# Kernel tuning notes

Measured on AMD Instinct MI355X. Metric: run time of the kernel, lower is better.

Reference implementation:

```python
import jax, jax.numpy as jnp
import numpy as np

E = 768   # embed_size
H = 64    # head_embed_size
B = 8
T = 4096  # == ctx_size


def setup_inputs() -> dict:
    key = jax.random.key(0)
    k1, k2, k3, k4 = jax.random.split(key, 4)
    inputs = jax.random.normal(k1, (B, T, E), dtype=jnp.float32)
    # Linear weights stored as (E, H) so projection is x @ W
    scale = 1.0 / np.sqrt(E)
    Wq = jax.random.uniform(k2, (E, H), dtype=jnp.float32, minval=-scale, maxval=scale)
    Wk = jax.random.uniform(k3, (E, H), dtype=jnp.float32, minval=-scale, maxval=scale)
    Wv = jax.random.uniform(k4, (E, H), dtype=jnp.float32, minval=-scale, maxval=scale)
    return {"inputs": inputs, "Wq": Wq, "Wk": Wk, "Wv": Wv}


def reference(inputs, Wq, Wk, Wv):
    Tlen = inputs.shape[1]
    q = inputs @ Wq  # (B,T,H)
    k = inputs @ Wk  # (B,T,H)
    v = inputs @ Wv  # (B,T,H)
    # NOTE: original module does NOT scale by 1/sqrt(H) — faithful reproduction.
    scores = jnp.einsum('bqh,bkh->bqk', q, k)  # (B,T,T)
    causal = jnp.tril(jnp.ones((Tlen, Tlen), dtype=bool))
    scores = jnp.where(causal, scores, -jnp.inf)
    attn = jax.nn.softmax(scores, axis=-1)
    # dropout=0 -> identity
    out = jnp.einsum('bqk,bkh->bqh', attn, v)  # (B,T,H)
    return out
```

## Files before the change

kernel.cpp:

```cpp
#include <hip/hip_runtime.h>
#include <hip/hip_bf16.h>

#define E_DIM 768
#define H_DIM 64
#define B_SZ 8
#define T_SZ 4096
#define BT (B_SZ * T_SZ)

typedef __attribute__((ext_vector_type(8))) short short8;
typedef __attribute__((ext_vector_type(4))) float floatx4;

#define RAWBAR() __asm__ volatile("s_waitcnt lgkmcnt(0)\n\ts_barrier" ::: "memory")

static __device__ __forceinline__ unsigned short bf1(float a) {
    __hip_bfloat16 h = __float2bfloat16(a);
    unsigned short u; __builtin_memcpy(&u, &h, 2); return u;
}
static __device__ __forceinline__ unsigned int pk2(float a, float b) {
    __hip_bfloat162 h = __float22bfloat162_rn(float2{a, b});
    unsigned int u; __builtin_memcpy(&u, &h, 4); return u;
}

__global__ __launch_bounds__(256) void prep_w(
    const float* __restrict__ Wq, const float* __restrict__ Wk,
    const float* __restrict__ Wv, unsigned short* __restrict__ Wt)
{
    __shared__ float Ls[64][65];
    const int nt = blockIdx.x;
    const int kc = blockIdx.y;
    const float* __restrict__ W = (nt == 0) ? Wq : (nt == 1) ? Wk : Wv;
    const float scl = (nt == 0) ? 1.44269504088896f : 1.0f;
    const int t = threadIdx.x;
    const int k0 = kc * 64;

#pragma unroll
    for (int it = 0; it < 16; ++it) {
        const int kk = (t >> 6) + it * 4;
        Ls[kk][t & 63] = W[(size_t)(k0 + kk) * H_DIM + (t & 63)];
    }
    __syncthreads();

#pragma unroll
    for (int it = 0; it < 4; ++it) {
        const int nl = (t >> 4) + it * 16;
        const int kl = (t & 15) * 4;
        unsigned int u[2];
        u[0] = pk2(Ls[kl + 0][nl] * scl, Ls[kl + 1][nl] * scl);
        u[1] = pk2(Ls[kl + 2][nl] * scl, Ls[kl + 3][nl] * scl);
        *(uint2*)(Wt + (size_t)(nt * 64 + nl) * E_DIM + k0 + kl) = *(uint2*)u;
    }
}

__global__ __launch_bounds__(768) void proj_mfma(
    const float* __restrict__ X, const unsigned short* __restrict__ Wt,
    unsigned short* __restrict__ Qb, unsigned short* __restrict__ Kb,
    unsigned short* __restrict__ Vtb)
{
    __shared__ unsigned short Xs[2][16][776];

    const int tid  = threadIdx.x;
    const int wave = tid >> 6, lane = tid & 63;
    const int row  = lane & 15, quad = lane >> 4;
    const int m0   = blockIdx.x * 128;

    short8 bfr[24];
    {
        const unsigned short* wp = Wt + (size_t)(wave * 16 + row) * E_DIM + quad * 8;
#pragma unroll
        for (int ks = 0; ks < 24; ++ks) bfr[ks] = *(const short8*)(wp + ks * 32);
    }

    const int srow = tid & 15;
    const int sc   = tid >> 4;
    const float* __restrict__ xbase = X + (size_t)(m0 + srow) * E_DIM + sc * 16;

    float4 fx[4];
#define LDX(mt)                                                               \
    {                                                                         \
        const float* p = xbase + (size_t)(mt) * 16 * E_DIM;                   \
        fx[0] = *(const float4*)(p);     fx[1] = *(const float4*)(p + 4);     \
        fx[2] = *(const float4*)(p + 8); fx[3] = *(const float4*)(p + 12);    \
    }
#define STX(buf)                                                              \
    {                                                                         \
        unsigned int tmp[8];                                                  \
        tmp[0] = pk2(fx[0].x, fx[0].y); tmp[1] = pk2(fx[0].z, fx[0].w);       \
        tmp[2] = pk2(fx[1].x, fx[1].y); tmp[3] = pk2(fx[1].z, fx[1].w);       \
        tmp[4] = pk2(fx[2].x, fx[2].y); tmp[5] = pk2(fx[2].z, fx[2].w);       \
        tmp[6] = pk2(fx[3].x, fx[3].y); tmp[7] = pk2(fx[3].z, fx[3].w);       \
        *(int4*)&Xs[buf][srow][sc * 16]     = *(int4*)&tmp[0];                \
        *(int4*)&Xs[buf][srow][sc * 16 + 8] = *(int4*)&tmp[4];                \
    }

    LDX(0); STX(0); LDX(1);
    RAWBAR();

    const int g  = wave >> 2;
    const int h  = (wave & 3) * 16 + row;
    unsigned short* __restrict__ OQK = (g == 0) ? Qb : Kb;
    const int bb = m0 >> 12;

    int cur = 0;
    for (int mt = 0; mt < 8; ++mt) {
        if (mt < 7) STX(cur ^ 1);
        if (mt < 6) LDX(mt + 2);

        floatx4 a0 = (floatx4)0.0f, a1 = (floatx4)0.0f;
        floatx4 a2 = (floatx4)0.0f, a3 = (floatx4)0.0f;
#pragma unroll
        for (int ks = 0; ks < 6; ++ks) {
            const short8 f0 = *(const short8*)&Xs[cur][row][(ks * 4 + 0) * 32 + quad * 8];
            const short8 f1 = *(const short8*)&Xs[cur][row][(ks * 4 + 1) * 32 + quad * 8];
            const short8 f2 = *(const short8*)&Xs[cur][row][(ks * 4 + 2) * 32 + quad * 8];
            const short8 f3 = *(const short8*)&Xs[cur][row][(ks * 4 + 3) * 32 + quad * 8];
            a0 = __builtin_amdgcn_mfma_f32_16x16x32_bf16(f0, bfr[ks * 4 + 0], a0, 0, 0, 0);
            a1 = __builtin_amdgcn_mfma_f32_16x16x32_bf16(f1, bfr[ks * 4 + 1], a1, 0, 0, 0);
            a2 = __builtin_amdgcn_mfma_f32_16x16x32_bf16(f2, bfr[ks * 4 + 2], a2, 0, 0, 0);
            a3 = __builtin_amdgcn_mfma_f32_16x16x32_bf16(f3, bfr[ks * 4 + 3], a3, 0, 0, 0);
        }
        floatx4 acc;
#pragma unroll
        for (int r = 0; r < 4; ++r) acc[r] = (a0[r] + a1[r]) + (a2[r] + a3[r]);

        const int mr = m0 + mt * 16 + quad * 4;
        if (g < 2) {
#pragma unroll
            for (int r = 0; r < 4; ++r)
                OQK[(size_t)(mr + r) * H_DIM + h] = bf1(acc[r]);
        } else {
            const int t0 = mr & 4095;
            unsigned int u[2];
            u[0] = pk2(acc[0], acc[1]); u[1] = pk2(acc[2], acc[3]);
            *(uint2*)(Vtb + ((size_t)bb * H_DIM + h) * T_SZ + t0) = *(uint2*)u;
        }

        RAWBAR();
        cur ^= 1;
    }
#undef LDX
#undef STX
}

__global__ __launch_bounds__(256, 6) void attn_mfma(
    const unsigned short* __restrict__ Qb,
    const unsigned short* __restrict__ Kb,
    const unsigned short* __restrict__ Vtb,
    float* __restrict__ Opart, float* __restrict__ lpart,
    float* __restrict__ Out)
{
    __shared__ __align__(16) unsigned short KV[2][64][72];
    __shared__ float lc[4][16];

    const int lb = blockIdx.x;
    const int b  = lb & 7;
    const int s  = lb >> 3;
    int qq, c, m;
    if (s < 128)      { m = 4; qq = 96 + (s >> 2); c = s & 3; }
    else if (s < 224) { m = 3; const int t = s - 128; const int t3 = t / 3; qq = 64 + t3; c = t - t3 * 3; }
    else if (s < 288) { m = 2; const int t = s - 224; qq = 32 + (t >> 1); c = t & 1; }
    else              { m = 1; qq = s - 288; c = 0; }
    const int ntot = (qq >> 1) + 1;
    const int k0t  = (c * ntot) / m;
    const int k1t  = ((c + 1) * ntot) / m;
    const int ktd  = ntot - 1;
    const int n    = k1t - k0t;
    const bool split = (m > 1);

    const int tid  = threadIdx.x;
    const int wave = tid >> 6, lane = tid & 63;
    const int col  = lane & 15, quad = lane >> 4;
    const int wq   = wave >> 1;
    const int wk   = wave & 1;

    const size_t base = (size_t)b * T_SZ * H_DIM;
    const int q0  = qq * 32;

    short8 qf0, qf1;
    {
        const unsigned short* qp = Qb + base + (size_t)(q0 + wq * 16 + col) * H_DIM + quad * 8;
        qf0 = *(const short8*)(qp);
        qf1 = *(const short8*)(qp + 32);
    }

    floatx4 o[4];
#pragma unroll
    for (int i = 0; i < 4; ++i) o[i] = (floatx4)0.0f;
    float lp = 0.0f;

    const int krow = tid >> 2, kcol = (tid & 3) * 16;
    const int kprow = (krow & 32) + ((krow >> 2) & 1) * 16 + ((krow & 31) >> 3) * 4 + (krow & 3);
    const unsigned short* __restrict__ Ksrc = Kb + base + (size_t)krow * H_DIM + kcol;
    const unsigned short* __restrict__ Vsrc = Vtb + ((size_t)b * H_DIM + krow) * T_SZ + kcol;

    int4 kr0, kr1, vr0, vr1;
#define LDKV(t)                                                          \
    {                                                                    \
        const unsigned short* kp = Ksrc + (size_t)(t) * 64 * H_DIM;      \
        kr0 = *(const int4*)kp; kr1 = *(const int4*)(kp + 8);            \
        const unsigned short* vp = Vsrc + (t) * 64;                      \
        vr0 = *(const int4*)vp; vr1 = *(const int4*)(vp + 8);            \
    }
#define STKV()                                                           \
    {                                                                    \
        *(int4*)&KV[0][kprow][kcol] = kr0; *(int4*)&KV[0][kprow][kcol + 8] = kr1; \
        *(int4*)&KV[1][krow][kcol] = vr0; *(int4*)&KV[1][krow][kcol + 8] = vr1; \
    }

    LDKV(k0t);
    STKV();
    if (n > 1) LDKV(k0t + 1);
    RAWBAR();

    for (int i = 0; i < n; ++i) {
        const int kt = k0t + i;

        floatx4 a0 = (floatx4)0.0f, a1 = (floatx4)0.0f;
        __builtin_amdgcn_s_setprio(1);
        {
            const unsigned short* kp0 = &KV[0][wk * 32 + col][quad * 8];
            const unsigned short* kp1 = &KV[0][wk * 32 + 16 + col][quad * 8];
            a0 = __builtin_amdgcn_mfma_f32_16x16x32_bf16(*(const short8*)(kp0),      qf0, a0, 0, 0, 0);
            a1 = __builtin_amdgcn_mfma_f32_16x16x32_bf16(*(const short8*)(kp1),      qf0, a1, 0, 0, 0);
            a0 = __builtin_amdgcn_mfma_f32_16x16x32_bf16(*(const short8*)(kp0 + 32), qf1, a0, 0, 0, 0);
            a1 = __builtin_amdgcn_mfma_f32_16x16x32_bf16(*(const short8*)(kp1 + 32), qf1, a1, 0, 0, 0);
        }
        __builtin_amdgcn_s_setprio(0);

        if (kt == ktd) {
            const int qg = q0 + wq * 16 + col;
            const int kb = kt * 64 + wk * 32 + quad * 8;
#pragma unroll
            for (int r = 0; r < 4; ++r) {
                if (kb + r > qg)     a0[r] = -1e30f;
                if (kb + 4 + r > qg) a1[r] = -1e30f;
            }
        }

        const float p0 = exp2f(a0[0]), p1 = exp2f(a0[1]), p2 = exp2f(a0[2]), p3 = exp2f(a0[3]);
        const float p4 = exp2f(a1[0]), p5 = exp2f(a1[1]), p6 = exp2f(a1[2]), p7 = exp2f(a1[3]);
        lp += ((p0 + p1) + (p2 + p3)) + ((p4 + p5) + (p6 + p7));
        unsigned int u0, u1, u2, u3;
        __asm__("v_cvt_pk_bf16_f32 %0, %1, %2" : "=v"(u0) : "v"(p0), "v"(p1));
        __asm__("v_cvt_pk_bf16_f32 %0, %1, %2" : "=v"(u1) : "v"(p2), "v"(p3));
        __asm__("v_cvt_pk_bf16_f32 %0, %1, %2" : "=v"(u2) : "v"(p4), "v"(p5));
        __asm__("v_cvt_pk_bf16_f32 %0, %1, %2" : "=v"(u3) : "v"(p6), "v"(p7));
        union { unsigned int u[4]; short8 v; } pu;
        pu.u[0] = u0; pu.u[1] = u1; pu.u[2] = u2; pu.u[3] = u3;
        const short8 pa = pu.v;

        __builtin_amdgcn_s_setprio(1);
#pragma unroll
        for (int d = 0; d < 4; ++d) {
            const short8 vb = *(const short8*)(&KV[1][d * 16 + col][wk * 32 + quad * 8]);
            o[d] = __builtin_amdgcn_mfma_f32_16x16x32_bf16(pa, vb, o[d], 0, 0, 0);
        }
        __builtin_amdgcn_s_setprio(0);

        RAWBAR();
        if (i + 1 < n) {
            STKV();
            if (i + 2 < n) LDKV(kt + 2);
        }
        RAWBAR();
    }

    lp += __shfl_xor(lp, 16);
    lp += __shfl_xor(lp, 32);
    if (quad == 0) lc[wave][col] = lp;
    __syncthreads();

    float* __restrict__ Oc = (float*)&KV[0][0][0];
#pragma unroll
    for (int r = 0; r < 4; ++r)
#pragma unroll
        for (int d = 0; d < 4; ++d)
            Oc[((wave * 16) + quad * 4 + r) * 64 + d * 16 + col] = o[d][r];
    __syncthreads();

    {
        const int orow = tid >> 3;
        const int d0   = (tid & 7) * 8;
        const int rl   = orow & 15;
        const int wb   = (orow >> 4) * 2;
        const float* p0 = &Oc[((wb * 16) + rl) * 64 + d0];
        const float* p1 = &Oc[(((wb + 1) * 16) + rl) * 64 + d0];
        const float lsum = lc[wb][rl] + lc[wb + 1][rl];
        float4 a0 = *(const float4*)(p0);
        float4 a1 = *(const float4*)(p0 + 4);
        const float4 b0 = *(const float4*)(p1);
        const float4 b1 = *(const float4*)(p1 + 4);
        a0.x += b0.x; a0.y += b0.y; a0.z += b0.z; a0.w += b0.w;
        a1.x += b1.x; a1.y += b1.y; a1.z += b1.z; a1.w += b1.w;
        if (!split) {
            const float inv = 1.0f / lsum;
            a0.x *= inv; a0.y *= inv; a0.z *= inv; a0.w *= inv;
            a1.x *= inv; a1.y *= inv; a1.z *= inv; a1.w *= inv;
            float* op = Out + base + (size_t)(q0 + orow) * H_DIM + d0;
            *(float4*)(op)     = a0;
            *(float4*)(op + 4) = a1;
        } else {
            const int pidx = (b * 96 + (qq - 32)) * 4 + c;
            float* op = Opart + ((size_t)pidx * 32 + orow) * 64 + d0;
            *(float4*)(op)     = a0;
            *(float4*)(op + 4) = a1;
            if ((tid & 7) == 0) lpart[pidx * 32 + orow] = lsum;
        }
    }
#undef LDKV
#undef STKV
}

__global__ __launch_bounds__(256) void attn_combine(
    const float* __restrict__ Opart, const float* __restrict__ lpart,
    float* __restrict__ Out)
{
    const int qi  = blockIdx.x;
    const int b   = blockIdx.y;
    const int qq  = 32 + qi;
    const int m   = (qq < 64) ? 2 : (qq < 96) ? 3 : 4;
    const int tid = threadIdx.x;
    const int orow = tid >> 3;
    const int d0   = (tid & 7) * 8;
    const int p0   = (b * 96 + qi) * 4;

    float4 a0 = {0.f, 0.f, 0.f, 0.f}, a1 = {0.f, 0.f, 0.f, 0.f};
    float l = 0.0f;
    for (int j = 0; j < m; ++j) {
        const float* P = Opart + ((size_t)(p0 + j) * 32 + orow) * 64 + d0;
        const float4 b0 = *(const float4*)(P);
        const float4 b1 = *(const float4*)(P + 4);
        a0.x += b0.x; a0.y += b0.y; a0.z += b0.z; a0.w += b0.w;
        a1.x += b1.x; a1.y += b1.y; a1.z += b1.z; a1.w += b1.w;
        l += lpart[(p0 + j) * 32 + orow];
    }
    const float inv = 1.0f / l;
    a0.x *= inv; a0.y *= inv; a0.z *= inv; a0.w *= inv;
    a1.x *= inv; a1.y *= inv; a1.z *= inv; a1.w *= inv;

    float* op = Out + ((size_t)b * T_SZ + qq * 32 + orow) * H_DIM + d0;
    *(float4*)(op)     = a0;
    *(float4*)(op + 4) = a1;
}

extern "C" void kernel_launch(void* const* d_in, const int* in_sizes, int n_in,
                              void* d_out, int out_size, void* d_ws, size_t ws_size,
                              hipStream_t stream) {
    const float* X  = (const float*)d_in[0];
    const float* Wq = (const float*)d_in[1];
    const float* Wk = (const float*)d_in[2];
    const float* Wv = (const float*)d_in[3];

    unsigned short* Wt  = (unsigned short*)d_ws;
    unsigned short* Qb  = Wt + (size_t)192 * E_DIM;
    unsigned short* Kb  = Qb + (size_t)BT * H_DIM;
    unsigned short* Vtb = Kb + (size_t)BT * H_DIM;
    float* Opart = (float*)(Vtb + (size_t)BT * H_DIM);
    float* lpart = Opart + (size_t)3072 * 32 * 64;

    prep_w<<<dim3(3, 12), 256, 0, stream>>>(Wq, Wk, Wv, Wt);
    proj_mfma<<<256, 768, 0, stream>>>(X, Wt, Qb, Kb, Vtb);
    attn_mfma<<<2560, 256, 0, stream>>>(Qb, Kb, Vtb, Opart, lpart, (float*)d_out);
    attn_combine<<<dim3(96, 8), 256, 0, stream>>>(Opart, lpart, (float*)d_out);
}
```

Before: 214.1 us.

## Grow attention query tile to 64 rows with each wave covering the full key tile

Each block now handles 64 query rows instead of 32, and each of the four waves owns 16 query rows across the whole 64-key tile. Each K/V tile loaded into shared memory is therefore reused by twice as many queries, and the cross-wave LDS reduction of partial outputs and row sums goes away, since each wave writes its rows directly. The split-K schedule is rebuilt for 64 query tiles with up to 6 chunks, and the grid and combine kernel are resized to match. The trade-off is fewer blocks (1632), more per-wave work and registers, and a lower occupancy hint of 5.

```diff
diff --git a/kernel.cpp b/kernel.cpp
--- a/kernel.cpp
+++ b/kernel.cpp
@@ -141,7 +141,7 @@
 #undef STX
 }
 
-__global__ __launch_bounds__(256, 6) void attn_mfma(
+__global__ __launch_bounds__(256, 5) void attn_mfma(
     const unsigned short* __restrict__ Qb,
     const unsigned short* __restrict__ Kb,
     const unsigned short* __restrict__ Vtb,
@@ -149,17 +149,18 @@
     float* __restrict__ Out)
 {
     __shared__ __align__(16) unsigned short KV[2][64][72];
-    __shared__ float lc[4][16];
 
     const int lb = blockIdx.x;
     const int b  = lb & 7;
     const int s  = lb >> 3;
     int qq, c, m;
-    if (s < 128)      { m = 4; qq = 96 + (s >> 2); c = s & 3; }
-    else if (s < 224) { m = 3; const int t = s - 128; const int t3 = t / 3; qq = 64 + t3; c = t - t3 * 3; }
-    else if (s < 288) { m = 2; const int t = s - 224; qq = 32 + (t >> 1); c = t & 1; }
-    else              { m = 1; qq = s - 288; c = 0; }
-    const int ntot = (qq >> 1) + 1;
+    if (s < 24)       { m = 6; qq = 60 + s / 6;                        c = s % 6; }
+    else if (s < 84)  { m = 5; const int i = s - 24;  qq = 48 + i / 5;    c = i % 5; }
+    else if (s < 132) { m = 4; const int i = s - 84;  qq = 36 + (i >> 2); c = i & 3; }
+    else if (s < 168) { m = 3; const int i = s - 132; qq = 24 + i / 3;    c = i % 3; }
+    else if (s < 192) { m = 2; const int i = s - 168; qq = 12 + (i >> 1); c = i & 1; }
+    else              { m = 1; qq = s - 192; c = 0; }
+    const int ntot = qq + 1;
     const int k0t  = (c * ntot) / m;
     const int k1t  = ((c + 1) * ntot) / m;
     const int ktd  = ntot - 1;
@@ -167,13 +168,12 @@
     const bool split = (m > 1);
 
     const int tid  = threadIdx.x;
-    const int wave = tid >> 6, lane = tid & 63;
+    const int wq   = tid >> 6;
+    const int lane = tid & 63;
     const int col  = lane & 15, quad = lane >> 4;
-    const int wq   = wave >> 1;
-    const int wk   = wave & 1;
 
     const size_t base = (size_t)b * T_SZ * H_DIM;
-    const int q0  = qq * 32;
+    const int q0  = qq * 64;
 
     short8 qf0, qf1;
     {
@@ -214,47 +214,50 @@
     for (int i = 0; i < n; ++i) {
         const int kt = k0t + i;
 
-        floatx4 a0 = (floatx4)0.0f, a1 = (floatx4)0.0f;
-        __builtin_amdgcn_s_setprio(1);
-        {
-            const unsigned short* kp0 = &KV[0][wk * 32 + col][quad * 8];
-            const unsigned short* kp1 = &KV[0][wk * 32 + 16 + col][quad * 8];
-            a0 = __builtin_amdgcn_mfma_f32_16x16x32_bf16(*(const short8*)(kp0),      qf0, a0, 0, 0, 0);
-            a1 = __builtin_amdgcn_mfma_f32_16x16x32_bf16(*(const short8*)(kp1),      qf0, a1, 0, 0, 0);
-            a0 = __builtin_amdgcn_mfma_f32_16x16x32_bf16(*(const short8*)(kp0 + 32), qf1, a0, 0, 0, 0);
-            a1 = __builtin_amdgcn_mfma_f32_16x16x32_bf16(*(const short8*)(kp1 + 32), qf1, a1, 0, 0, 0);
-        }
-        __builtin_amdgcn_s_setprio(0);
-
-        if (kt == ktd) {
-            const int qg = q0 + wq * 16 + col;
-            const int kb = kt * 64 + wk * 32 + quad * 8;
-#pragma unroll
-            for (int r = 0; r < 4; ++r) {
-                if (kb + r > qg)     a0[r] = -1e30f;
-                if (kb + 4 + r > qg) a1[r] = -1e30f;
+#pragma unroll
+        for (int j = 0; j < 2; ++j) {
+            floatx4 a0 = (floatx4)0.0f, a1 = (floatx4)0.0f;
+            __builtin_amdgcn_s_setprio(1);
+            {
+                const unsigned short* kp0 = &KV[0][j * 32 + col][quad * 8];
+                const unsigned short* kp1 = &KV[0][j * 32 + 16 + col][quad * 8];
+                a0 = __builtin_amdgcn_mfma_f32_16x16x32_bf16(*(const short8*)(kp0),      qf0, a0, 0, 0, 0);
+                a1 = __builtin_amdgcn_mfma_f32_16x16x32_bf16(*(const short8*)(kp1),      qf0, a1, 0, 0, 0);
+                a0 = __builtin_amdgcn_mfma_f32_16x16x32_bf16(*(const short8*)(kp0 + 32), qf1, a0, 0, 0, 0);
+                a1 = __builtin_amdgcn_mfma_f32_16x16x32_bf16(*(const short8*)(kp1 + 32), qf1, a1, 0, 0, 0);
             }
-        }
-
-        const float p0 = exp2f(a0[0]), p1 = exp2f(a0[1]), p2 = exp2f(a0[2]), p3 = exp2f(a0[3]);
-        const float p4 = exp2f(a1[0]), p5 = exp2f(a1[1]), p6 = exp2f(a1[2]), p7 = exp2f(a1[3]);
-        lp += ((p0 + p1) + (p2 + p3)) + ((p4 + p5) + (p6 + p7));
-        unsigned int u0, u1, u2, u3;
-        __asm__("v_cvt_pk_bf16_f32 %0, %1, %2" : "=v"(u0) : "v"(p0), "v"(p1));
-        __asm__("v_cvt_pk_bf16_f32 %0, %1, %2" : "=v"(u1) : "v"(p2), "v"(p3));
-        __asm__("v_cvt_pk_bf16_f32 %0, %1, %2" : "=v"(u2) : "v"(p4), "v"(p5));
-        __asm__("v_cvt_pk_bf16_f32 %0, %1, %2" : "=v"(u3) : "v"(p6), "v"(p7));
-        union { unsigned int u[4]; short8 v; } pu;
-        pu.u[0] = u0; pu.u[1] = u1; pu.u[2] = u2; pu.u[3] = u3;
-        const short8 pa = pu.v;
-
-        __builtin_amdgcn_s_setprio(1);
-#pragma unroll
-        for (int d = 0; d < 4; ++d) {
-            const short8 vb = *(const short8*)(&KV[1][d * 16 + col][wk * 32 + quad * 8]);
-            o[d] = __builtin_amdgcn_mfma_f32_16x16x32_bf16(pa, vb, o[d], 0, 0, 0);
-        }
-        __builtin_amdgcn_s_setprio(0);
+            __builtin_amdgcn_s_setprio(0);
+
+            if (kt == ktd) {
+                const int qg = q0 + wq * 16 + col;
+                const int kb = kt * 64 + j * 32 + quad * 8;
+#pragma unroll
+                for (int r = 0; r < 4; ++r) {
+                    if (kb + r > qg)     a0[r] = -1e30f;
+                    if (kb + 4 + r > qg) a1[r] = -1e30f;
+                }
+            }
+
+            const float p0 = exp2f(a0[0]), p1 = exp2f(a0[1]), p2 = exp2f(a0[2]), p3 = exp2f(a0[3]);
+            const float p4 = exp2f(a1[0]), p5 = exp2f(a1[1]), p6 = exp2f(a1[2]), p7 = exp2f(a1[3]);
+            lp += ((p0 + p1) + (p2 + p3)) + ((p4 + p5) + (p6 + p7));
+            unsigned int u0, u1, u2, u3;
+            __asm__("v_cvt_pk_bf16_f32 %0, %1, %2" : "=v"(u0) : "v"(p0), "v"(p1));
+            __asm__("v_cvt_pk_bf16_f32 %0, %1, %2" : "=v"(u1) : "v"(p2), "v"(p3));
+            __asm__("v_cvt_pk_bf16_f32 %0, %1, %2" : "=v"(u2) : "v"(p4), "v"(p5));
+            __asm__("v_cvt_pk_bf16_f32 %0, %1, %2" : "=v"(u3) : "v"(p6), "v"(p7));
+            union { unsigned int u[4]; short8 v; } pu;
+            pu.u[0] = u0; pu.u[1] = u1; pu.u[2] = u2; pu.u[3] = u3;
+            const short8 pa = pu.v;
+
+            __builtin_amdgcn_s_setprio(1);
+#pragma unroll
+            for (int d = 0; d < 4; ++d) {
+                const short8 vb = *(const short8*)(&KV[1][d * 16 + col][j * 32 + quad * 8]);
+                o[d] = __builtin_amdgcn_mfma_f32_16x16x32_bf16(pa, vb, o[d], 0, 0, 0);
+            }
+            __builtin_amdgcn_s_setprio(0);
+        }
 
         RAWBAR();
         if (i + 1 < n) {
@@ -266,45 +269,28 @@
 
     lp += __shfl_xor(lp, 16);
     lp += __shfl_xor(lp, 32);
-    if (quad == 0) lc[wave][col] = lp;
-    __syncthreads();
-
-    float* __restrict__ Oc = (float*)&KV[0][0][0];
-#pragma unroll
-    for (int r = 0; r < 4; ++r)
-#pragma unroll
-        for (int d = 0; d < 4; ++d)
-            Oc[((wave * 16) + quad * 4 + r) * 64 + d * 16 + col] = o[d][r];
-    __syncthreads();
-
-    {
-        const int orow = tid >> 3;
-        const int d0   = (tid & 7) * 8;
-        const int rl   = orow & 15;
-        const int wb   = (orow >> 4) * 2;
-        const float* p0 = &Oc[((wb * 16) + rl) * 64 + d0];
-        const float* p1 = &Oc[(((wb + 1) * 16) + rl) * 64 + d0];
-        const float lsum = lc[wb][rl] + lc[wb + 1][rl];
-        float4 a0 = *(const float4*)(p0);
-        float4 a1 = *(const float4*)(p0 + 4);
-        const float4 b0 = *(const float4*)(p1);
-        const float4 b1 = *(const float4*)(p1 + 4);
-        a0.x += b0.x; a0.y += b0.y; a0.z += b0.z; a0.w += b0.w;
-        a1.x += b1.x; a1.y += b1.y; a1.z += b1.z; a1.w += b1.w;
-        if (!split) {
-            const float inv = 1.0f / lsum;
-            a0.x *= inv; a0.y *= inv; a0.z *= inv; a0.w *= inv;
-            a1.x *= inv; a1.y *= inv; a1.z *= inv; a1.w *= inv;
-            float* op = Out + base + (size_t)(q0 + orow) * H_DIM + d0;
-            *(float4*)(op)     = a0;
-            *(float4*)(op + 4) = a1;
-        } else {
-            const int pidx = (b * 96 + (qq - 32)) * 4 + c;
-            float* op = Opart + ((size_t)pidx * 32 + orow) * 64 + d0;
-            *(float4*)(op)     = a0;
-            *(float4*)(op + 4) = a1;
-            if ((tid & 7) == 0) lpart[pidx * 32 + orow] = lsum;
-        }
+    float lr[4];
+#pragma unroll
+    for (int r = 0; r < 4; ++r) lr[r] = __shfl(lp, quad * 4 + r);
+
+    if (!split) {
+        float* op = Out + base + (size_t)(q0 + wq * 16 + quad * 4) * H_DIM;
+#pragma unroll
+        for (int r = 0; r < 4; ++r) {
+            const float inv = 1.0f / lr[r];
+#pragma unroll
+            for (int d = 0; d < 4; ++d)
+                op[(size_t)r * H_DIM + d * 16 + col] = o[d][r] * inv;
+        }
+    } else {
+        const int pidx = (b * 64 + qq) * 6 + c;
+        float* op = Opart + ((size_t)pidx * 64 + wq * 16 + quad * 4) * 64;
+#pragma unroll
+        for (int r = 0; r < 4; ++r)
+#pragma unroll
+            for (int d = 0; d < 4; ++d)
+                op[(size_t)r * 64 + d * 16 + col] = o[d][r];
+        if (quad == 0) lpart[pidx * 64 + wq * 16 + col] = lp;
     }
 #undef LDKV
 #undef STKV
@@ -314,32 +300,40 @@
     const float* __restrict__ Opart, const float* __restrict__ lpart,
     float* __restrict__ Out)
 {
-    const int qi  = blockIdx.x;
+    const int qq  = 12 + blockIdx.x;
     const int b   = blockIdx.y;
-    const int qq  = 32 + qi;
-    const int m   = (qq < 64) ? 2 : (qq < 96) ? 3 : 4;
+    const int m   = (qq + 12) / 12;
     const int tid = threadIdx.x;
-    const int orow = tid >> 3;
-    const int d0   = (tid & 7) * 8;
-    const int p0   = (b * 96 + qi) * 4;
-
-    float4 a0 = {0.f, 0.f, 0.f, 0.f}, a1 = {0.f, 0.f, 0.f, 0.f};
+    const int orow = tid >> 2;
+    const int d0   = (tid & 3) * 16;
+    const int p0   = (b * 64 + qq) * 6;
+
+    float4 a0 = {0.f,0.f,0.f,0.f}, a1 = {0.f,0.f,0.f,0.f};
+    float4 a2 = {0.f,0.f,0.f,0.f}, a3 = {0.f,0.f,0.f,0.f};
     float l = 0.0f;
     for (int j = 0; j < m; ++j) {
-        const float* P = Opart + ((size_t)(p0 + j) * 32 + orow) * 64 + d0;
+        const float* P = Opart + ((size_t)(p0 + j) * 64 + orow) * 64 + d0;
         const float4 b0 = *(const float4*)(P);
         const float4 b1 = *(const float4*)(P + 4);
+        const float4 b2 = *(const float4*)(P + 8);
+        const float4 b3 = *(const float4*)(P + 12);
         a0.x += b0.x; a0.y += b0.y; a0.z += b0.z; a0.w += b0.w;
         a1.x += b1.x; a1.y += b1.y; a1.z += b1.z; a1.w += b1.w;
-        l += lpart[(p0 + j) * 32 + orow];
+        a2.x += b2.x; a2.y += b2.y; a2.z += b2.z; a2.w += b2.w;
+        a3.x += b3.x; a3.y += b3.y; a3.z += b3.z; a3.w += b3.w;
+        l += lpart[(p0 + j) * 64 + orow];
     }
     const float inv = 1.0f / l;
     a0.x *= inv; a0.y *= inv; a0.z *= inv; a0.w *= inv;
     a1.x *= inv; a1.y *= inv; a1.z *= inv; a1.w *= inv;
-
-    float* op = Out + ((size_t)b * T_SZ + qq * 32 + orow) * H_DIM + d0;
-    *(float4*)(op)     = a0;
-    *(float4*)(op + 4) = a1;
+    a2.x *= inv; a2.y *= inv; a2.z *= inv; a2.w *= inv;
+    a3.x *= inv; a3.y *= inv; a3.z *= inv; a3.w *= inv;
+
+    float* op = Out + ((size_t)b * T_SZ + qq * 64 + orow) * H_DIM + d0;
+    *(float4*)(op)      = a0;
+    *(float4*)(op + 4)  = a1;
+    *(float4*)(op + 8)  = a2;
+    *(float4*)(op + 12) = a3;
 }
 
 extern "C" void kernel_launch(void* const* d_in, const int* in_sizes, int n_in,
@@ -355,10 +349,10 @@
     unsigned short* Kb  = Qb + (size_t)BT * H_DIM;
     unsigned short* Vtb = Kb + (size_t)BT * H_DIM;
     float* Opart = (float*)(Vtb + (size_t)BT * H_DIM);
-    float* lpart = Opart + (size_t)3072 * 32 * 64;
+    float* lpart = Opart + (size_t)3072 * 64 * 64;
 
     prep_w<<<dim3(3, 12), 256, 0, stream>>>(Wq, Wk, Wv, Wt);
     proj_mfma<<<256, 768, 0, stream>>>(X, Wt, Qb, Kb, Vtb);
-    attn_mfma<<<2560, 256, 0, stream>>>(Qb, Kb, Vtb, Opart, lpart, (float*)d_out);
-    attn_combine<<<dim3(96, 8), 256, 0, stream>>>(Opart, lpart, (float*)d_out);
-}
+    attn_mfma<<<1632, 256, 0, stream>>>(Qb, Kb, Vtb, Opart, lpart, (float*)d_out);
+    attn_combine<<<dim3(52, 8), 256, 0, stream>>>(Opart, lpart, (float*)d_out);
+}
```

Result: no change. 212.0 us (median of 2 runs) (-1.0%).
